# Kernel optimization log

Hardware: AMD Instinct MI355X
Metric: run time of the kernel (lower is better)

Reference implementation:

```python
import jax, jax.numpy as jnp
import numpy as np

N = 12       # data qubits
NA = 1       # ancilla qubits
NTOT = N + NA
L = 6        # circuit layers
B = 512      # Ndata
DIM = 2 ** NTOT
DDATA = 2 ** N


def _cz_sign():
    # Combined diagonal sign of all CZ gates in one layer (CZs are diagonal and commute).
    idx = np.arange(DIM)
    bits = (idx[None, :] >> (NTOT - 1 - np.arange(NTOT))[:, None]) & 1  # [NTOT, DIM], qubit 0 = MSB
    sign = np.ones(DIM)
    for i in range(NTOT // 2):
        sign *= 1 - 2 * (bits[2 * i] * bits[2 * i + 1])
    for i in range((NTOT - 1) // 2):
        sign *= 1 - 2 * (bits[2 * i + 1] * bits[2 * i + 2])
    return jnp.asarray(sign, jnp.complex64)

_CZ_SIGN = _cz_sign()


def _apply_1q(state, U, q):
    # state: [B, DIM] complex; apply 2x2 U on qubit q (qubit 0 = most significant axis)
    left, right = 2 ** q, 2 ** (NTOT - 1 - q)
    s = state.reshape(-1, left, 2, right)
    s = jnp.einsum('ji,blir->bljr', U, s)
    return s.reshape(-1, DIM)


def _back_circuit(state, params):
    # hardware-efficient ansatz: per layer, RX+RY on every qubit then brickwork CZ
    for l in range(L):
        for q in range(NTOT):
            tx = params[2 * NTOT * l + q]
            ty = params[2 * NTOT * l + NTOT + q]
            cx = jnp.cos(tx / 2).astype(jnp.complex64)
            sx = jnp.sin(tx / 2).astype(jnp.complex64)
            cy = jnp.cos(ty / 2).astype(jnp.complex64)
            sy = jnp.sin(ty / 2).astype(jnp.complex64)
            RX = jnp.stack([jnp.stack([cx, -1j * sx]), jnp.stack([-1j * sx, cx])])
            RY = jnp.stack([jnp.stack([cy, -sy]), jnp.stack([sy, cy])])
            state = _apply_1q(state, RY @ RX, q)  # RX then RY, fused into one 2x2
        state = state * _CZ_SIGN
    return state


def setup_inputs() -> dict:
    key = jax.random.key(0)
    k1, k2, k3, k4 = jax.random.split(key, 4)
    re = jax.random.normal(k1, (B, DIM), dtype=jnp.float32)
    im = jax.random.normal(k2, (B, DIM), dtype=jnp.float32)
    # physical inputs: ancilla (qubit 0, MSB) in |0>, normalized state vectors
    mask = (jnp.arange(DIM) < DDATA).astype(jnp.float32)
    re = re * mask
    im = im * mask
    norm = jnp.sqrt(jnp.sum(re ** 2 + im ** 2, axis=1, keepdims=True))
    re = re / norm
    im = im / norm
    params = jax.random.normal(k3, (2 * NTOT * L,), dtype=jnp.float32)
    m_res = jax.random.randint(k4, (B,), 0, 2, dtype=jnp.int32)
    return {"inputs_re": re, "inputs_im": im, "params": params, "m_res": m_res}


def reference(inputs_re, inputs_im, params, m_res):
    # backwardOutput_t with mseq=False: circuit, then measure ancilla (outcome m_res),
    # post-select and renormalize. Output as stacked (real, imag): [B, 2**n, 2].
    state = (inputs_re + 1j * inputs_im).astype(jnp.complex64)
    out = _back_circuit(state, params)
    post = jnp.where((m_res == 0)[:, None], out[:, :DDATA], out[:, DDATA:])
    norm = jnp.sqrt(jnp.sum(jnp.abs(post) ** 2, axis=1, keepdims=True))
    post = post / norm
    return jnp.stack([post.real, post.imag], axis=-1)
```

## Files before the change

### kernel.cpp

```cpp
#include <hip/hip_runtime.h>

constexpr int NTOT   = 13;
constexpr int DIM    = 1 << NTOT;
constexpr int DDATA  = DIM / 2;
constexpr int LAYERS = 6;
constexpr int NGATES = LAYERS * NTOT;
constexpr int BLOCK  = 1024;

__global__ void gates_precompute(const float* __restrict__ params,
                                 float* __restrict__ gates) {
    int t = threadIdx.x;
    if (t >= NGATES) return;
    int l = t / NTOT, q = t % NTOT;
    float tx = params[2 * NTOT * l + q];
    float ty = params[2 * NTOT * l + NTOT + q];
    float sx, cx, sy, cy;
    sincosf(0.5f * tx, &sx, &cx);
    sincosf(0.5f * ty, &sy, &cy);
    gates[4 * t + 0] = cy * cx;
    gates[4 * t + 1] = sy * sx;
    gates[4 * t + 2] = sy * cx;
    gates[4 * t + 3] = cy * sx;
}

__device__ __forceinline__ int swz(int idx) { return idx ^ (((idx >> 4) & 7) << 1); }

__device__ __forceinline__ void gate_pair(float2& va, float2& vb,
                                          float A, float B, float C, float D) {
    float ar = va.x, ai = va.y, br = vb.x, bi = vb.y;
    va.x = A * ar - B * ai - C * br + D * bi;
    va.y = B * ar + A * ai - D * br - C * bi;
    vb.x = C * ar + D * ai + A * br + B * bi;
    vb.y = C * ai - D * ar + A * bi - B * br;
}

template<int S, bool LAST>
__device__ __forceinline__ void do_pass(float2* s, const float* __restrict__ g,
                                        int l, int qbase, int p) {
    const int base = ((p >> S) << (S + 3)) | (p & ((1 << S) - 1));
    float2 v[8];
    int addr[8];
    #pragma unroll
    for (int m = 0; m < 8; ++m) {
        addr[m] = swz(base | (m << S));
        v[m] = s[addr[m]];
    }
    #pragma unroll
    for (int c = 0; c < 3; ++c) {
        const float* gp = g + 4 * (l * NTOT + qbase + c);
        const float A = gp[0], B = gp[1], C = gp[2], D = gp[3];
        const int lb = 4 >> c;
        #pragma unroll
        for (int m = 0; m < 8; ++m)
            if (!(m & lb)) gate_pair(v[m], v[m | lb], A, B, C, D);
    }
    if (LAST) {
        const float* gp = g + 4 * (l * NTOT + 12);
        const float A = gp[0], B = gp[1], C = gp[2], D = gp[3];
        const int odd = p & 1;
        const float Bs = odd ? -B : B;
        const float Cq = odd ? C : -C;
        #pragma unroll
        for (int m = 0; m < 8; ++m) {
            float vr = v[m].x, vi = v[m].y;
            float pr = __shfl_xor(vr, 1, 64);
            float pi = __shfl_xor(vi, 1, 64);
            float nr = A * vr - Bs * vi + Cq * pr + D * pi;
            float ni = A * vi + Bs * vr + Cq * pi - D * pr;
            int idx = base | (m << S);
            float sg = 1.0f - 2.0f * (float)(__popc(idx & (idx >> 1)) & 1);
            v[m].x = nr * sg;
            v[m].y = ni * sg;
        }
    }
    #pragma unroll
    for (int m = 0; m < 8; ++m) s[addr[m]] = v[m];
}

__global__ __launch_bounds__(BLOCK)
void qddpm_main(const float* __restrict__ re_in, const float* __restrict__ im_in,
                const int* __restrict__ m_res, const float* __restrict__ g,
                float* __restrict__ out) {
    __shared__ float2 s[DIM];
    const int b = blockIdx.x;
    const int t = threadIdx.x;

    const float4* re4 = reinterpret_cast<const float4*>(re_in + (size_t)b * DIM);
    const float4* im4 = reinterpret_cast<const float4*>(im_in + (size_t)b * DIM);
    #pragma unroll
    for (int k = 0; k < DIM / 4 / BLOCK; ++k) {
        int e = t + k * BLOCK;
        float4 r = re4[e];
        float4 i = im4[e];
        s[swz(4 * e + 0)] = make_float2(r.x, i.x);
        s[swz(4 * e + 1)] = make_float2(r.y, i.y);
        s[swz(4 * e + 2)] = make_float2(r.z, i.z);
        s[swz(4 * e + 3)] = make_float2(r.w, i.w);
    }
    __syncthreads();

    for (int l = 0; l < LAYERS; ++l) {
        do_pass<10, false>(s, g, l, 0, t); __syncthreads();
        do_pass<7,  false>(s, g, l, 3, t); __syncthreads();
        do_pass<4,  false>(s, g, l, 6, t); __syncthreads();
        do_pass<1,  true >(s, g, l, 9, t); __syncthreads();
    }

    const int off = (m_res[b] == 0) ? 0 : DDATA;
    float2 v[4];
    float acc = 0.f;
    #pragma unroll
    for (int u = 0; u < 4; ++u) {
        v[u] = s[swz(off + 4 * t + u)];
        acc += v[u].x * v[u].x + v[u].y * v[u].y;
    }
    #pragma unroll
    for (int o = 32; o > 0; o >>= 1) acc += __shfl_down(acc, o, 64);
    __syncthreads();
    float* red = reinterpret_cast<float*>(s);
    if ((t & 63) == 0) red[t >> 6] = acc;
    __syncthreads();
    if (t == 0) {
        float tot = 0.f;
        #pragma unroll
        for (int w = 0; w < BLOCK / 64; ++w) tot += red[w];
        red[16] = rsqrtf(tot);
    }
    __syncthreads();
    const float sc = red[16];
    float4* o4 = reinterpret_cast<float4*>(out + (size_t)b * DDATA * 2);
    o4[2 * t + 0] = make_float4(v[0].x * sc, v[0].y * sc, v[1].x * sc, v[1].y * sc);
    o4[2 * t + 1] = make_float4(v[2].x * sc, v[2].y * sc, v[3].x * sc, v[3].y * sc);
}

extern "C" void kernel_launch(void* const* d_in, const int* in_sizes, int n_in,
                              void* d_out, int out_size, void* d_ws, size_t ws_size,
                              hipStream_t stream) {
    const float* re     = (const float*)d_in[0];
    const float* im     = (const float*)d_in[1];
    const float* params = (const float*)d_in[2];
    const int*   mres   = (const int*)d_in[3];
    float* out   = (float*)d_out;
    float* gates = (float*)d_ws;

    const int B = in_sizes[3];

    gates_precompute<<<1, 128, 0, stream>>>(params, gates);
    qddpm_main<<<B, BLOCK, 0, stream>>>(re, im, mres, gates, out);
}
```

Before: 186.8 us.

## Restructure layer into two shared-memory passes with 16 amplitudes per thread and shuffles

Each thread now holds 16 amplitudes instead of 8 and uses a 512-thread block. Each layer applies 4 gates in registers, 5 gates through wavefront shuffles, then one shared-memory transpose and 4 more gates. The aim is to cut shared-memory round trips and barriers from four per layer to two, with a new XOR swizzle to avoid bank conflicts. The cost is more register pressure, many cross-lane shuffles, and fewer threads per block. The final normalization and output also read directly from registers, and only the post-selected half writes.

```diff
diff --git a/kernel.cpp b/kernel.cpp
--- a/kernel.cpp
+++ b/kernel.cpp
@@ -5,7 +5,7 @@
 constexpr int DDATA  = DIM / 2;
 constexpr int LAYERS = 6;
 constexpr int NGATES = LAYERS * NTOT;
-constexpr int BLOCK  = 1024;
+constexpr int BLOCK  = 512;
 
 __global__ void gates_precompute(const float* __restrict__ params,
                                  float* __restrict__ gates) {
@@ -23,7 +23,7 @@
     gates[4 * t + 3] = cy * sx;
 }
 
-__device__ __forceinline__ int swz(int idx) { return idx ^ (((idx >> 4) & 7) << 1); }
+__device__ __forceinline__ int phi(int idx) { return idx ^ ((idx >> 4) & 15); }
 
 __device__ __forceinline__ void gate_pair(float2& va, float2& vb,
                                           float A, float B, float C, float D) {
@@ -34,103 +34,127 @@
     vb.y = C * ai - D * ar + A * bi - B * br;
 }
 
-template<int S, bool LAST>
-__device__ __forceinline__ void do_pass(float2* s, const float* __restrict__ g,
-                                        int l, int qbase, int p) {
-    const int base = ((p >> S) << (S + 3)) | (p & ((1 << S) - 1));
-    float2 v[8];
-    int addr[8];
-    #pragma unroll
-    for (int m = 0; m < 8; ++m) {
-        addr[m] = swz(base | (m << S));
-        v[m] = s[addr[m]];
-    }
-    #pragma unroll
-    for (int c = 0; c < 3; ++c) {
-        const float* gp = g + 4 * (l * NTOT + qbase + c);
-        const float A = gp[0], B = gp[1], C = gp[2], D = gp[3];
-        const int lb = 4 >> c;
-        #pragma unroll
-        for (int m = 0; m < 8; ++m)
-            if (!(m & lb)) gate_pair(v[m], v[m | lb], A, B, C, D);
-    }
-    if (LAST) {
-        const float* gp = g + 4 * (l * NTOT + 12);
-        const float A = gp[0], B = gp[1], C = gp[2], D = gp[3];
-        const int odd = p & 1;
-        const float Bs = odd ? -B : B;
-        const float Cq = odd ? C : -C;
-        #pragma unroll
-        for (int m = 0; m < 8; ++m) {
-            float vr = v[m].x, vi = v[m].y;
-            float pr = __shfl_xor(vr, 1, 64);
-            float pi = __shfl_xor(vi, 1, 64);
-            float nr = A * vr - Bs * vi + Cq * pr + D * pi;
-            float ni = A * vi + Bs * vr + Cq * pi - D * pr;
-            int idx = base | (m << S);
-            float sg = 1.0f - 2.0f * (float)(__popc(idx & (idx >> 1)) & 1);
-            v[m].x = nr * sg;
-            v[m].y = ni * sg;
-        }
-    }
-    #pragma unroll
-    for (int m = 0; m < 8; ++m) s[addr[m]] = v[m];
-}
-
-__global__ __launch_bounds__(BLOCK)
+__global__ __launch_bounds__(BLOCK, 4)
 void qddpm_main(const float* __restrict__ re_in, const float* __restrict__ im_in,
                 const int* __restrict__ m_res, const float* __restrict__ g,
                 float* __restrict__ out) {
     __shared__ float2 s[DIM];
     const int b = blockIdx.x;
     const int t = threadIdx.x;
+    const int L = t & 63;
+    const int w = t >> 6;
 
     const float4* re4 = reinterpret_cast<const float4*>(re_in + (size_t)b * DIM);
     const float4* im4 = reinterpret_cast<const float4*>(im_in + (size_t)b * DIM);
     #pragma unroll
-    for (int k = 0; k < DIM / 4 / BLOCK; ++k) {
+    for (int k = 0; k < 4; ++k) {
         int e = t + k * BLOCK;
         float4 r = re4[e];
         float4 i = im4[e];
-        s[swz(4 * e + 0)] = make_float2(r.x, i.x);
-        s[swz(4 * e + 1)] = make_float2(r.y, i.y);
-        s[swz(4 * e + 2)] = make_float2(r.z, i.z);
-        s[swz(4 * e + 3)] = make_float2(r.w, i.w);
+        s[phi(4 * e + 0)] = make_float2(r.x, i.x);
+        s[phi(4 * e + 1)] = make_float2(r.y, i.y);
+        s[phi(4 * e + 2)] = make_float2(r.z, i.z);
+        s[phi(4 * e + 3)] = make_float2(r.w, i.w);
     }
     __syncthreads();
 
+    const int baseA = (L << 3) | w;
+    const int addrA = phi(baseA);
+    const int baseB = (w << 10) | (L << 4);
+    int addrB[16];
+    #pragma unroll
+    for (int m = 0; m < 16; ++m) addrB[m] = baseB | (m ^ (L & 15));
+
+    float2 v[16];
+
     for (int l = 0; l < LAYERS; ++l) {
-        do_pass<10, false>(s, g, l, 0, t); __syncthreads();
-        do_pass<7,  false>(s, g, l, 3, t); __syncthreads();
-        do_pass<4,  false>(s, g, l, 6, t); __syncthreads();
-        do_pass<1,  true >(s, g, l, 9, t); __syncthreads();
+        const float* gl = g + 4 * NTOT * l;
+
+        #pragma unroll
+        for (int m = 0; m < 16; ++m) v[m] = s[addrA + (m << 9)];
+
+        #pragma unroll
+        for (int q = 0; q < 4; ++q) {
+            const float A = gl[4 * q], B = gl[4 * q + 1];
+            const float C = gl[4 * q + 2], D = gl[4 * q + 3];
+            const int bit = 8 >> q;
+            #pragma unroll
+            for (int m = 0; m < 16; ++m)
+                if (!(m & bit)) gate_pair(v[m], v[m | bit], A, B, C, D);
+        }
+
+        #pragma unroll
+        for (int q = 4; q < 9; ++q) {
+            const float A = gl[4 * q], B = gl[4 * q + 1];
+            const float C = gl[4 * q + 2], D = gl[4 * q + 3];
+            const int sh = 9 - q;
+            const int xm = 1 << sh;
+            const int bit = (L >> sh) & 1;
+            const float Bs = bit ? -B : B;
+            const float Cq = bit ? C : -C;
+            #pragma unroll
+            for (int m = 0; m < 16; ++m) {
+                float vr = v[m].x, vi = v[m].y;
+                float pr = __shfl_xor(vr, xm, 64);
+                float pi = __shfl_xor(vi, xm, 64);
+                v[m].x = A * vr - Bs * vi + Cq * pr + D * pi;
+                v[m].y = A * vi + Bs * vr + Cq * pi - D * pr;
+            }
+        }
+
+        #pragma unroll
+        for (int m = 0; m < 16; ++m) s[addrA + (m << 9)] = v[m];
+        __syncthreads();
+        #pragma unroll
+        for (int m = 0; m < 16; ++m) v[m] = s[addrB[m]];
+
+        #pragma unroll
+        for (int q = 9; q < 13; ++q) {
+            const float A = gl[4 * q], B = gl[4 * q + 1];
+            const float C = gl[4 * q + 2], D = gl[4 * q + 3];
+            const int bit = 8 >> (q - 9);
+            #pragma unroll
+            for (int m = 0; m < 16; ++m)
+                if (!(m & bit)) gate_pair(v[m], v[m | bit], A, B, C, D);
+        }
+
+        #pragma unroll
+        for (int m = 0; m < 16; ++m) {
+            int idx = baseB | m;
+            float sg = 1.0f - 2.0f * (float)(__popc(idx & (idx >> 1)) & 1);
+            v[m].x *= sg;
+            v[m].y *= sg;
+        }
+
+        if (l < LAYERS - 1) {
+            #pragma unroll
+            for (int m = 0; m < 16; ++m) s[addrB[m]] = v[m];
+            __syncthreads();
+        }
     }
 
-    const int off = (m_res[b] == 0) ? 0 : DDATA;
-    float2 v[4];
-    float acc = 0.f;
+    const int keep = (m_res[b] != 0) ? 1 : 0;
+    const bool mine = ((w >> 2) & 1) == keep;
+    float acc = 0.0f;
     #pragma unroll
-    for (int u = 0; u < 4; ++u) {
-        v[u] = s[swz(off + 4 * t + u)];
-        acc += v[u].x * v[u].x + v[u].y * v[u].y;
-    }
+    for (int m = 0; m < 16; ++m) acc += v[m].x * v[m].x + v[m].y * v[m].y;
     #pragma unroll
     for (int o = 32; o > 0; o >>= 1) acc += __shfl_down(acc, o, 64);
     __syncthreads();
     float* red = reinterpret_cast<float*>(s);
-    if ((t & 63) == 0) red[t >> 6] = acc;
+    if (L == 0) red[w] = acc;
     __syncthreads();
-    if (t == 0) {
-        float tot = 0.f;
+    const float tot = red[keep * 4 + 0] + red[keep * 4 + 1]
+                    + red[keep * 4 + 2] + red[keep * 4 + 3];
+    const float sc = rsqrtf(tot);
+    if (mine) {
+        const int j = ((w & 3) << 10) | (L << 4);
+        float4* o4 = reinterpret_cast<float4*>(out + (size_t)b * DDATA * 2 + (size_t)j * 2);
         #pragma unroll
-        for (int w = 0; w < BLOCK / 64; ++w) tot += red[w];
-        red[16] = rsqrtf(tot);
+        for (int m = 0; m < 8; ++m)
+            o4[m] = make_float4(v[2 * m].x * sc, v[2 * m].y * sc,
+                                v[2 * m + 1].x * sc, v[2 * m + 1].y * sc);
     }
-    __syncthreads();
-    const float sc = red[16];
-    float4* o4 = reinterpret_cast<float4*>(out + (size_t)b * DDATA * 2);
-    o4[2 * t + 0] = make_float4(v[0].x * sc, v[0].y * sc, v[1].x * sc, v[1].y * sc);
-    o4[2 * t + 1] = make_float4(v[2].x * sc, v[2].y * sc, v[3].x * sc, v[3].y * sc);
 }
 
 extern "C" void kernel_launch(void* const* d_in, const int* in_sizes, int n_in,
```

Result: slower. 237.5 us (+27.1%).
